# Performance work log

Hardware: AMD Instinct MI355X
Metric: run time of the kernel (lower is better)

The kernel has to match this reference:

```python
import jax, jax.numpy as jnp
import numpy as np

N_NODES = 100000
N_EDGES = 1600000
DIM = 128
BN_EPS = 1e-5


def setup_inputs() -> dict:
    key = jax.random.key(0)
    k1, k2, k3, k4 = jax.random.split(key, 4)
    scale = 1.0 / np.sqrt(DIM)
    return {
        "x": jax.random.normal(k1, (N_NODES, DIM), dtype=jnp.float32),
        "edge_index": jax.random.randint(k2, (2, N_EDGES), 0, N_NODES, dtype=jnp.int64),
        "W_l": jax.random.normal(k3, (DIM, DIM), dtype=jnp.float32) * scale,
        "b_l": jnp.zeros((DIM,), dtype=jnp.float32),
        "W_r": jax.random.normal(k4, (DIM, DIM), dtype=jnp.float32) * scale,
        "gamma": jnp.ones((DIM,), dtype=jnp.float32),
        "beta": jnp.zeros((DIM,), dtype=jnp.float32),
    }


def reference(x, edge_index, W_l, b_l, W_r, gamma, beta):
    n = x.shape[0]
    src, dst = edge_index[0], edge_index[1]
    # SAGEConv mean aggregation: gather source features, scatter-sum to dst, divide by degree
    agg = jax.ops.segment_sum(x[src], dst, num_segments=n)          # [N, d_in]
    deg = jax.ops.segment_sum(jnp.ones_like(src, dtype=x.dtype), dst, num_segments=n)
    mean = agg / jnp.maximum(deg, 1.0)[:, None]
    # lin_l(mean) + lin_r(x)  (bias lives in lin_l, PyG default)
    h = mean @ W_l + b_l + x @ W_r                                   # [N, d_out]
    # act -> BatchNorm1d (training mode, batch stats) -> dropout(p=0, identity)
    h = jax.nn.relu(h)
    mu = jnp.mean(h, axis=0)
    var = jnp.mean(jnp.square(h - mu), axis=0)                       # biased var, as torch BN
    h = (h - mu) * jax.lax.rsqrt(var + BN_EPS) * gamma + beta
    # residual
    return x + h
```

## Files before the change

### kernel.cpp

```cpp
#include <hip/hip_runtime.h>

#define DIM 128
#define BN_EPS 1e-5f
#define NB 32
#define NBK_MAX 512

typedef __attribute__((ext_vector_type(8))) short bf16x8;
typedef __attribute__((ext_vector_type(4))) float f32x4;

union B8 { uint4 u; bf16x8 s; };

__device__ __forceinline__ ushort f2bf(float f) {
    unsigned u = __float_as_uint(f);
    u += 0x7fffu + ((u >> 16) & 1u);
    return (ushort)(u >> 16);
}

__global__ void k_prep(const float4* __restrict__ x4, const float* __restrict__ Wl,
                       const float* __restrict__ Wr, const unsigned* __restrict__ eiu,
                       int* __restrict__ bcnt, uint2* __restrict__ xf8,
                       uint4* __restrict__ wpack, int nn, int ne, int PB, int WB) {
    __shared__ int nz;
    __shared__ int lh[NBK_MAX];
    int b = blockIdx.x;
    const int tid = threadIdx.x;

    if (b < PB) {
        const int t = b * 256 + tid;
        const int n8 = nn * DIM / 8;
        if (t < n8) {
            const float4 a = x4[2 * t], c = x4[2 * t + 1];
            int u0 = __builtin_amdgcn_cvt_pk_fp8_f32(a.x, a.y, 0, false);
            u0 = __builtin_amdgcn_cvt_pk_fp8_f32(a.z, a.w, u0, true);
            int u1 = __builtin_amdgcn_cvt_pk_fp8_f32(c.x, c.y, 0, false);
            u1 = __builtin_amdgcn_cvt_pk_fp8_f32(c.z, c.w, u1, true);
            xf8[t] = make_uint2((unsigned)u0, (unsigned)u1);
        }
        return;
    }
    b -= PB;
    if (b < WB) {
        const int t = b * 256 + tid;
        const int lane = t & 63, kk = (t >> 6) & 3, nt = (t >> 8) & 7, mat = t >> 11;
        const float* W = mat ? Wr : Wl;
        const int k0 = kk * 32 + (lane >> 4) * 8;
        const int n = nt * 16 + (lane & 15);
        ushort e[8];
#pragma unroll
        for (int j = 0; j < 8; ++j) e[j] = f2bf(W[(size_t)(k0 + j) * DIM + n]);
        uint4 o;
        o.x = ((unsigned)e[1] << 16) | e[0];
        o.y = ((unsigned)e[3] << 16) | e[2];
        o.z = ((unsigned)e[5] << 16) | e[4];
        o.w = ((unsigned)e[7] << 16) | e[6];
        wpack[t] = o;
        return;
    }
    b -= WB;
    const int nbk = (nn + 255) >> 8;
    for (int i = tid; i < nbk; i += 256) lh[i] = 0;
    if (tid == 0) nz = 0;
    __syncthreads();
    const int e0 = b * 4096;
    {
        int es = e0 + tid * 16;
        if (es >= ne) es = ne - 1;
        if (eiu[2 * (size_t)es + 1] != 0) atomicOr(&nz, 1);
    }
    __syncthreads();
    const int is64 = (nz == 0);
    for (int j = 0; j < 16; ++j) {
        const int e = e0 + j * 256 + tid;
        if (e < ne) {
            int dst;
            if (is64) dst = (int)((const long long*)eiu)[(size_t)ne + e];
            else      dst = ((const int*)eiu)[(size_t)ne + e];
            atomicAdd(&lh[dst >> 8], 1);
        }
    }
    __syncthreads();
    for (int i = tid; i < nbk; i += 256)
        if (lh[i]) atomicAdd(&bcnt[i], lh[i]);
}

__global__ __launch_bounds__(512) void k_scanb(const int* __restrict__ bcnt,
                                               int* __restrict__ bbase,
                                               int* __restrict__ cursor2, int nn, int ne) {
    __shared__ int sd[512];
    const int nbk = (nn + 255) >> 8;
    const int tid = threadIdx.x;
    const int v = (tid < nbk) ? bcnt[tid] : 0;
    sd[tid] = v;
    __syncthreads();
    for (int ofs = 1; ofs < 512; ofs <<= 1) {
        const int t = (tid >= ofs) ? sd[tid - ofs] : 0;
        __syncthreads();
        sd[tid] += t;
        __syncthreads();
    }
    if (tid < nbk) {
        const int ex = sd[tid] - v;
        bbase[tid] = ex;
        cursor2[tid] = ex;
    }
    if (tid == 0) bbase[nbk] = ne;
}

__global__ __launch_bounds__(256) void k_passA(const unsigned* __restrict__ eiu,
                                               int* __restrict__ cursor2,
                                               unsigned* __restrict__ pairbuf,
                                               int nn, int ne) {
    __shared__ int lh[NBK_MAX];
    __shared__ int gb[NBK_MAX];
    __shared__ int nz;
    const int nbk = (nn + 255) >> 8;
    const int tid = threadIdx.x;
    const int e0 = blockIdx.x * 4096;
    for (int i = tid; i < nbk; i += 256) lh[i] = 0;
    if (tid == 0) nz = 0;
    __syncthreads();
    {
        int es = e0 + tid * 16;
        if (es >= ne) es = ne - 1;
        if (eiu[2 * (size_t)es + 1] != 0) atomicOr(&nz, 1);
    }
    __syncthreads();
    const int is64 = (nz == 0);
    unsigned pay[16];
    int bkrank[16];
#pragma unroll
    for (int j = 0; j < 16; ++j) {
        const int e = e0 + j * 256 + tid;
        bkrank[j] = -1;
        if (e < ne) {
            int src, dst;
            if (is64) {
                const long long* p = (const long long*)eiu;
                src = (int)p[e];
                dst = (int)p[(size_t)ne + e];
            } else {
                const int* p = (const int*)eiu;
                src = p[e];
                dst = p[(size_t)ne + e];
            }
            const int bk = dst >> 8;
            const int rank = atomicAdd(&lh[bk], 1);
            bkrank[j] = (bk << 16) | rank;
            pay[j] = ((unsigned)(dst & 255) << 24) | (unsigned)src;
        }
    }
    __syncthreads();
    for (int i = tid; i < nbk; i += 256) {
        const int c = lh[i];
        gb[i] = c ? atomicAdd(&cursor2[i], c) : 0;
    }
    __syncthreads();
#pragma unroll
    for (int j = 0; j < 16; ++j) {
        if (bkrank[j] >= 0) {
            const int bk = bkrank[j] >> 16, rank = bkrank[j] & 0xFFFF;
            pairbuf[gb[bk] + rank] = pay[j];
        }
    }
}

__global__ __launch_bounds__(256) void k_passB(const unsigned* __restrict__ pairbuf,
                                               const int* __restrict__ bbase,
                                               int* __restrict__ off, int* __restrict__ cnt,
                                               int* __restrict__ srcbuf, int nn) {
    __shared__ int cl[256];
    __shared__ int sd[256];
    __shared__ int cur[256];
    const int tid = threadIdx.x;
    const int b = blockIdx.x;
    const int node0 = b << 8;
    const int e0 = bbase[b], e1 = bbase[b + 1];
    cl[tid] = 0;
    __syncthreads();
    for (int e = e0 + tid; e < e1; e += 256)
        atomicAdd(&cl[pairbuf[e] >> 24], 1);
    __syncthreads();
    const int v = cl[tid];
    sd[tid] = v;
    __syncthreads();
    for (int ofs = 1; ofs < 256; ofs <<= 1) {
        const int t = (tid >= ofs) ? sd[tid - ofs] : 0;
        __syncthreads();
        sd[tid] += t;
        __syncthreads();
    }
    const int ex = sd[tid] - v;
    cur[tid] = ex;
    const int node = node0 + tid;
    if (node < nn) {
        off[node] = e0 + ex;
        cnt[node] = v;
    }
    __syncthreads();
    for (int e = e0 + tid; e < e1; e += 256) {
        const unsigned p = pairbuf[e];
        const int pos = atomicAdd(&cur[p >> 24], 1);
        srcbuf[e0 + pos] = (int)(p & 0xFFFFFFu);
    }
}

__global__ __launch_bounds__(512, 4) void k_gemm(
    const float* __restrict__ x, const uint2* __restrict__ xf8,
    const uint4* __restrict__ wpack, const float* __restrict__ bl,
    const int* __restrict__ off, const int* __restrict__ cnt,
    const int* __restrict__ srcbuf,
    ushort* __restrict__ hout, float* __restrict__ ssum, float* __restrict__ ssq,
    int nn)
{
    __shared__ uint4 mean4[NB * 16];
    __shared__ uint4 xls4[NB * 16];
    __shared__ float red_sum[2][DIM];
    __shared__ float red_sq[2][DIM];
    unsigned* x_u = (unsigned*)xls4;

    const int tid = threadIdx.x;
    const int lane = tid & 63;
    const int w = tid >> 6;
    const int base = blockIdx.x * NB;
    const int g16 = lane >> 4;
    const int q = lane & 15;

    for (int n = 0; n < 4; ++n) {
        const int ln = w * 4 + n;
        const int node = base + ln;
        float acc[8];
#pragma unroll
        for (int j = 0; j < 8; ++j) acc[j] = 0.f;
        unsigned xw = 0;

        if (node < nn) {
            const float2 xv = *(const float2*)(x + (size_t)node * DIM + 2 * lane);
            xw = ((unsigned)f2bf(xv.y) << 16) | f2bf(xv.x);

            const int o = off[node];
            const int c = cnt[node];
            int e = 0;
            for (; e + 8 <= c; e += 8) {
                const int s0 = srcbuf[o + e + g16];
                const int s1 = srcbuf[o + e + 4 + g16];
                const uint2 v0 = xf8[(size_t)s0 * 16 + q];
                const uint2 v1 = xf8[(size_t)s1 * 16 + q];
                {
                    auto p0 = __builtin_amdgcn_cvt_pk_f32_fp8(v0.x, false);
                    auto p1 = __builtin_amdgcn_cvt_pk_f32_fp8(v0.x, true);
                    auto p2 = __builtin_amdgcn_cvt_pk_f32_fp8(v0.y, false);
                    auto p3 = __builtin_amdgcn_cvt_pk_f32_fp8(v0.y, true);
                    acc[0] += p0[0]; acc[1] += p0[1]; acc[2] += p1[0]; acc[3] += p1[1];
                    acc[4] += p2[0]; acc[5] += p2[1]; acc[6] += p3[0]; acc[7] += p3[1];
                }
                {
                    auto p0 = __builtin_amdgcn_cvt_pk_f32_fp8(v1.x, false);
                    auto p1 = __builtin_amdgcn_cvt_pk_f32_fp8(v1.x, true);
                    auto p2 = __builtin_amdgcn_cvt_pk_f32_fp8(v1.y, false);
                    auto p3 = __builtin_amdgcn_cvt_pk_f32_fp8(v1.y, true);
                    acc[0] += p0[0]; acc[1] += p0[1]; acc[2] += p1[0]; acc[3] += p1[1];
                    acc[4] += p2[0]; acc[5] += p2[1]; acc[6] += p3[0]; acc[7] += p3[1];
                }
            }
            for (; e + 4 <= c; e += 4) {
                const int s = srcbuf[o + e + g16];
                const uint2 v = xf8[(size_t)s * 16 + q];
                auto p0 = __builtin_amdgcn_cvt_pk_f32_fp8(v.x, false);
                auto p1 = __builtin_amdgcn_cvt_pk_f32_fp8(v.x, true);
                auto p2 = __builtin_amdgcn_cvt_pk_f32_fp8(v.y, false);
                auto p3 = __builtin_amdgcn_cvt_pk_f32_fp8(v.y, true);
                acc[0] += p0[0]; acc[1] += p0[1]; acc[2] += p1[0]; acc[3] += p1[1];
                acc[4] += p2[0]; acc[5] += p2[1]; acc[6] += p3[0]; acc[7] += p3[1];
            }
            const int rem = c - e;
            if (g16 < rem) {
                const int s = srcbuf[o + e + g16];
                const uint2 v = xf8[(size_t)s * 16 + q];
                auto p0 = __builtin_amdgcn_cvt_pk_f32_fp8(v.x, false);
                auto p1 = __builtin_amdgcn_cvt_pk_f32_fp8(v.x, true);
                auto p2 = __builtin_amdgcn_cvt_pk_f32_fp8(v.y, false);
                auto p3 = __builtin_amdgcn_cvt_pk_f32_fp8(v.y, true);
                acc[0] += p0[0]; acc[1] += p0[1]; acc[2] += p1[0]; acc[3] += p1[1];
                acc[4] += p2[0]; acc[5] += p2[1]; acc[6] += p3[0]; acc[7] += p3[1];
            }
#pragma unroll
            for (int j = 0; j < 8; ++j) {
                acc[j] += __shfl_xor(acc[j], 16);
                acc[j] += __shfl_xor(acc[j], 32);
            }
            const float r = 1.0f / fmaxf((float)c, 1.0f);
#pragma unroll
            for (int j = 0; j < 8; ++j) acc[j] *= r;
        }

        const int sw = (((lane >> 2) ^ (ln & 15)) << 2) | (lane & 3);
        x_u[ln * 64 + sw] = xw;
        if (lane < 16) {
            uint4 mp;
            mp.x = ((unsigned)f2bf(acc[1]) << 16) | f2bf(acc[0]);
            mp.y = ((unsigned)f2bf(acc[3]) << 16) | f2bf(acc[2]);
            mp.z = ((unsigned)f2bf(acc[5]) << 16) | f2bf(acc[4]);
            mp.w = ((unsigned)f2bf(acc[7]) << 16) | f2bf(acc[6]);
            mean4[ln * 16 + (q ^ (ln & 15))] = mp;
        }
    }
    __syncthreads();

    const int m = w & 1;
    const int nh = w >> 1;
    const int row16 = lane & 15;
    const int kgrp = lane >> 4;
    const int ln2 = m * 16 + row16;

    bf16x8 am[4], ax[4];
#pragma unroll
    for (int kk = 0; kk < 4; ++kk) {
        const int unit = (kk * 4 + kgrp) ^ row16;
        B8 va, vb;
        va.u = mean4[ln2 * 16 + unit];
        vb.u = xls4[ln2 * 16 + unit];
        am[kk] = va.s;
        ax[kk] = vb.s;
    }

    f32x4 acc[2];
#pragma unroll
    for (int j = 0; j < 2; ++j) {
        const float bv = bl[(nh * 2 + j) * 16 + row16];
        acc[j] = (f32x4){bv, bv, bv, bv};
    }

#pragma unroll
    for (int j = 0; j < 2; ++j) {
        const int nt = nh * 2 + j;
        const uint4* pl = wpack + (size_t)(nt * 4) * 64 + lane;
        const uint4* pr = wpack + (size_t)((8 + nt) * 4) * 64 + lane;
        B8 wl[4], wr[4];
#pragma unroll
        for (int kk = 0; kk < 4; ++kk) {
            wl[kk].u = pl[kk * 64];
            wr[kk].u = pr[kk * 64];
        }
#pragma unroll
        for (int kk = 0; kk < 4; ++kk)
            acc[j] = __builtin_amdgcn_mfma_f32_16x16x32_bf16(am[kk], wl[kk].s, acc[j], 0, 0, 0);
#pragma unroll
        for (int kk = 0; kk < 4; ++kk)
            acc[j] = __builtin_amdgcn_mfma_f32_16x16x32_bf16(ax[kk], wr[kk].s, acc[j], 0, 0, 0);
    }

#pragma unroll
    for (int j = 0; j < 2; ++j) {
        const int feat = (nh * 2 + j) * 16 + row16;
        float s = 0.f, sq = 0.f;
#pragma unroll
        for (int r = 0; r < 4; ++r) {
            const int node = base + m * 16 + kgrp * 4 + r;
            const float v = fmaxf(acc[j][r], 0.0f);
            if (node < nn) {
                hout[(size_t)node * DIM + feat] = f2bf(v);
                s += v;
                sq += v * v;
            }
        }
        s += __shfl_xor(s, 16);
        s += __shfl_xor(s, 32);
        sq += __shfl_xor(sq, 16);
        sq += __shfl_xor(sq, 32);
        if (lane < 16) {
            red_sum[m][feat] = s;
            red_sq[m][feat] = sq;
        }
    }
    __syncthreads();
    if (tid < DIM) {
        atomicAdd(&ssum[tid], red_sum[0][tid] + red_sum[1][tid]);
        atomicAdd(&ssq[tid], red_sq[0][tid] + red_sq[1][tid]);
    }
}

__global__ void k_finalize(const float* __restrict__ x, const uint4* __restrict__ h8,
                           const float* __restrict__ ssum, const float* __restrict__ ssq,
                           const float* __restrict__ gamma, const float* __restrict__ beta,
                           float* __restrict__ out, int nn)
{
    const float invN = 1.0f / (float)nn;
    const int total8 = nn * DIM / 8;
    const int stride = gridDim.x * blockDim.x;
    for (int i = blockIdx.x * blockDim.x + threadIdx.x; i < total8; i += stride) {
        const int f4 = 2 * (i & 15);
        const uint4 hv = h8[i];
        const float4 xa = ((const float4*)x)[2 * i];
        const float4 xb = ((const float4*)x)[2 * i + 1];
        const float4 s4a = ((const float4*)ssum)[f4], s4b = ((const float4*)ssum)[f4 + 1];
        const float4 q4a = ((const float4*)ssq)[f4], q4b = ((const float4*)ssq)[f4 + 1];
        const float4 g4a = ((const float4*)gamma)[f4], g4b = ((const float4*)gamma)[f4 + 1];
        const float4 b4a = ((const float4*)beta)[f4], b4b = ((const float4*)beta)[f4 + 1];
        float h[8];
        h[0] = __uint_as_float(hv.x << 16);
        h[1] = __uint_as_float(hv.x & 0xffff0000u);
        h[2] = __uint_as_float(hv.y << 16);
        h[3] = __uint_as_float(hv.y & 0xffff0000u);
        h[4] = __uint_as_float(hv.z << 16);
        h[5] = __uint_as_float(hv.z & 0xffff0000u);
        h[6] = __uint_as_float(hv.w << 16);
        h[7] = __uint_as_float(hv.w & 0xffff0000u);
        float4 oa, ob;
        {
            const float mu = s4a.x * invN, rs = rsqrtf(q4a.x * invN - mu * mu + BN_EPS);
            oa.x = xa.x + (h[0] - mu) * rs * g4a.x + b4a.x;
        }
        {
            const float mu = s4a.y * invN, rs = rsqrtf(q4a.y * invN - mu * mu + BN_EPS);
            oa.y = xa.y + (h[1] - mu) * rs * g4a.y + b4a.y;
        }
        {
            const float mu = s4a.z * invN, rs = rsqrtf(q4a.z * invN - mu * mu + BN_EPS);
            oa.z = xa.z + (h[2] - mu) * rs * g4a.z + b4a.z;
        }
        {
            const float mu = s4a.w * invN, rs = rsqrtf(q4a.w * invN - mu * mu + BN_EPS);
            oa.w = xa.w + (h[3] - mu) * rs * g4a.w + b4a.w;
        }
        {
            const float mu = s4b.x * invN, rs = rsqrtf(q4b.x * invN - mu * mu + BN_EPS);
            ob.x = xb.x + (h[4] - mu) * rs * g4b.x + b4b.x;
        }
        {
            const float mu = s4b.y * invN, rs = rsqrtf(q4b.y * invN - mu * mu + BN_EPS);
            ob.y = xb.y + (h[5] - mu) * rs * g4b.y + b4b.y;
        }
        {
            const float mu = s4b.z * invN, rs = rsqrtf(q4b.z * invN - mu * mu + BN_EPS);
            ob.z = xb.z + (h[6] - mu) * rs * g4b.z + b4b.z;
        }
        {
            const float mu = s4b.w * invN, rs = rsqrtf(q4b.w * invN - mu * mu + BN_EPS);
            ob.w = xb.w + (h[7] - mu) * rs * g4b.w + b4b.w;
        }
        ((float4*)out)[2 * i] = oa;
        ((float4*)out)[2 * i + 1] = ob;
    }
}

extern "C" void kernel_launch(void* const* d_in, const int* in_sizes, int n_in,
                              void* d_out, int out_size, void* d_ws, size_t ws_size,
                              hipStream_t stream) {
    const float* x     = (const float*)d_in[0];
    const void*  ei    = d_in[1];
    const float* Wl    = (const float*)d_in[2];
    const float* bl    = (const float*)d_in[3];
    const float* Wr    = (const float*)d_in[4];
    const float* gamma = (const float*)d_in[5];
    const float* beta  = (const float*)d_in[6];
    float* out = (float*)d_out;

    const int nn = in_sizes[0] / DIM;
    const int ne = in_sizes[1] / 2;
    const int nbk = (nn + 255) >> 8;

    int* ws = (int*)d_ws;
    int*   bcnt    = ws;
    float* ssum    = (float*)(ws + 512);
    float* ssq     = (float*)(ws + 640);
    int*   bbase   = ws + 768;
    int*   cursor2 = ws + 1280;
    int*   cnt     = ws + 1792;
    int*   off     = cnt + nn;
    size_t pos = 1792 + 2 * (size_t)nn;
    pos = (pos + 3) & ~(size_t)3;
    uint4* wpack  = (uint4*)(ws + pos);
    int*   srcbuf = (int*)(wpack + 4096);
    size_t p2 = (size_t)(srcbuf + ne - ws);
    p2 = (p2 + 3) & ~(size_t)3;
    uint2* xf8 = (uint2*)(ws + p2);
    unsigned* pairbuf = (unsigned*)(xf8 + (size_t)nn * 16);
    ushort*   hbuf    = (ushort*)pairbuf;

    hipMemsetAsync(d_ws, 0, 768 * sizeof(int), stream);

    const int PB = (nn * DIM / 8 + 255) / 256;
    const int WB = 16;
    const int HB = (ne + 4095) / 4096;
    k_prep<<<PB + WB + HB, 256, 0, stream>>>((const float4*)x, Wl, Wr,
                                             (const unsigned*)ei, bcnt, xf8, wpack,
                                             nn, ne, PB, WB);
    k_scanb<<<1, 512, 0, stream>>>(bcnt, bbase, cursor2, nn, ne);
    k_passA<<<(ne + 4095) / 4096, 256, 0, stream>>>((const unsigned*)ei, cursor2,
                                                    pairbuf, nn, ne);
    k_passB<<<nbk, 256, 0, stream>>>(pairbuf, bbase, off, cnt, srcbuf, nn);
    k_gemm<<<(nn + NB - 1) / NB, 512, 0, stream>>>(x, xf8, wpack, bl, off, cnt, srcbuf,
                                                   hbuf, ssum, ssq, nn);
    k_finalize<<<2048, 256, 0, stream>>>(x, (const uint4*)hbuf, ssum, ssq, gamma, beta,
                                         out, nn);
}
```

Measured before the change: 194.2 us.

## Assign one node per 16-lane group in aggregation and per-node finalize grid

The neighbour-gather phase of k_gemm now maps each 16-lane quarter-wave to its own node, so a wave handles four nodes at once. Previously the whole wave walked one node at a time, with the four quarters splitting its edges and a cross-lane shuffle reduction at the end. This drops the shuffle reduction and the serial four-node loop, but spreads uneven degrees across lanes in the same wave, so divergence rises. The x tile is packed to bf16 in uint4 chunks per lane, and k_finalize switches from a grid-stride loop to one block per 32-node tile.

```diff
diff --git a/kernel.cpp b/kernel.cpp
--- a/kernel.cpp
+++ b/kernel.cpp
@@ -205,7 +205,7 @@
 }
 
 __global__ __launch_bounds__(512, 4) void k_gemm(
-    const float* __restrict__ x, const uint2* __restrict__ xf8,
+    const float4* __restrict__ x4g, const uint2* __restrict__ xf8,
     const uint4* __restrict__ wpack, const float* __restrict__ bl,
     const int* __restrict__ off, const int* __restrict__ cnt,
     const int* __restrict__ srcbuf,
@@ -216,55 +216,56 @@
     __shared__ uint4 xls4[NB * 16];
     __shared__ float red_sum[2][DIM];
     __shared__ float red_sq[2][DIM];
-    unsigned* x_u = (unsigned*)xls4;
 
     const int tid = threadIdx.x;
     const int lane = tid & 63;
     const int w = tid >> 6;
     const int base = blockIdx.x * NB;
-    const int g16 = lane >> 4;
+    const int g = lane >> 4;
     const int q = lane & 15;
 
-    for (int n = 0; n < 4; ++n) {
-        const int ln = w * 4 + n;
+    {
+        const int ln = w * 4 + g;
         const int node = base + ln;
         float acc[8];
 #pragma unroll
         for (int j = 0; j < 8; ++j) acc[j] = 0.f;
-        unsigned xw = 0;
+        uint4 xp = make_uint4(0, 0, 0, 0);
 
         if (node < nn) {
-            const float2 xv = *(const float2*)(x + (size_t)node * DIM + 2 * lane);
-            xw = ((unsigned)f2bf(xv.y) << 16) | f2bf(xv.x);
+            const float4 xa = x4g[(size_t)node * 32 + 2 * q];
+            const float4 xb = x4g[(size_t)node * 32 + 2 * q + 1];
+            xp.x = ((unsigned)f2bf(xa.y) << 16) | f2bf(xa.x);
+            xp.y = ((unsigned)f2bf(xa.w) << 16) | f2bf(xa.z);
+            xp.z = ((unsigned)f2bf(xb.y) << 16) | f2bf(xb.x);
+            xp.w = ((unsigned)f2bf(xb.w) << 16) | f2bf(xb.z);
 
             const int o = off[node];
             const int c = cnt[node];
             int e = 0;
-            for (; e + 8 <= c; e += 8) {
-                const int s0 = srcbuf[o + e + g16];
-                const int s1 = srcbuf[o + e + 4 + g16];
-                const uint2 v0 = xf8[(size_t)s0 * 16 + q];
-                const uint2 v1 = xf8[(size_t)s1 * 16 + q];
-                {
-                    auto p0 = __builtin_amdgcn_cvt_pk_f32_fp8(v0.x, false);
-                    auto p1 = __builtin_amdgcn_cvt_pk_f32_fp8(v0.x, true);
-                    auto p2 = __builtin_amdgcn_cvt_pk_f32_fp8(v0.y, false);
-                    auto p3 = __builtin_amdgcn_cvt_pk_f32_fp8(v0.y, true);
-                    acc[0] += p0[0]; acc[1] += p0[1]; acc[2] += p1[0]; acc[3] += p1[1];
-                    acc[4] += p2[0]; acc[5] += p2[1]; acc[6] += p3[0]; acc[7] += p3[1];
-                }
-                {
-                    auto p0 = __builtin_amdgcn_cvt_pk_f32_fp8(v1.x, false);
-                    auto p1 = __builtin_amdgcn_cvt_pk_f32_fp8(v1.x, true);
-                    auto p2 = __builtin_amdgcn_cvt_pk_f32_fp8(v1.y, false);
-                    auto p3 = __builtin_amdgcn_cvt_pk_f32_fp8(v1.y, true);
+            for (; e + 4 <= c; e += 4) {
+                const int s0 = srcbuf[o + e + 0];
+                const int s1 = srcbuf[o + e + 1];
+                const int s2 = srcbuf[o + e + 2];
+                const int s3 = srcbuf[o + e + 3];
+                const uint2 v0 = xf8[(unsigned)(s0 * 16 + q)];
+                const uint2 v1 = xf8[(unsigned)(s1 * 16 + q)];
+                const uint2 v2 = xf8[(unsigned)(s2 * 16 + q)];
+                const uint2 v3 = xf8[(unsigned)(s3 * 16 + q)];
+#pragma unroll
+                for (int k = 0; k < 4; ++k) {
+                    const uint2 v = (k == 0) ? v0 : (k == 1) ? v1 : (k == 2) ? v2 : v3;
+                    auto p0 = __builtin_amdgcn_cvt_pk_f32_fp8(v.x, false);
+                    auto p1 = __builtin_amdgcn_cvt_pk_f32_fp8(v.x, true);
+                    auto p2 = __builtin_amdgcn_cvt_pk_f32_fp8(v.y, false);
+                    auto p3 = __builtin_amdgcn_cvt_pk_f32_fp8(v.y, true);
                     acc[0] += p0[0]; acc[1] += p0[1]; acc[2] += p1[0]; acc[3] += p1[1];
                     acc[4] += p2[0]; acc[5] += p2[1]; acc[6] += p3[0]; acc[7] += p3[1];
                 }
             }
-            for (; e + 4 <= c; e += 4) {
-                const int s = srcbuf[o + e + g16];
-                const uint2 v = xf8[(size_t)s * 16 + q];
+            for (; e < c; ++e) {
+                const int s = srcbuf[o + e];
+                const uint2 v = xf8[(unsigned)(s * 16 + q)];
                 auto p0 = __builtin_amdgcn_cvt_pk_f32_fp8(v.x, false);
                 auto p1 = __builtin_amdgcn_cvt_pk_f32_fp8(v.x, true);
                 auto p2 = __builtin_amdgcn_cvt_pk_f32_fp8(v.y, false);
@@ -272,37 +273,19 @@
                 acc[0] += p0[0]; acc[1] += p0[1]; acc[2] += p1[0]; acc[3] += p1[1];
                 acc[4] += p2[0]; acc[5] += p2[1]; acc[6] += p3[0]; acc[7] += p3[1];
             }
-            const int rem = c - e;
-            if (g16 < rem) {
-                const int s = srcbuf[o + e + g16];
-                const uint2 v = xf8[(size_t)s * 16 + q];
-                auto p0 = __builtin_amdgcn_cvt_pk_f32_fp8(v.x, false);
-                auto p1 = __builtin_amdgcn_cvt_pk_f32_fp8(v.x, true);
-                auto p2 = __builtin_amdgcn_cvt_pk_f32_fp8(v.y, false);
-                auto p3 = __builtin_amdgcn_cvt_pk_f32_fp8(v.y, true);
-                acc[0] += p0[0]; acc[1] += p0[1]; acc[2] += p1[0]; acc[3] += p1[1];
-                acc[4] += p2[0]; acc[5] += p2[1]; acc[6] += p3[0]; acc[7] += p3[1];
-            }
-#pragma unroll
-            for (int j = 0; j < 8; ++j) {
-                acc[j] += __shfl_xor(acc[j], 16);
-                acc[j] += __shfl_xor(acc[j], 32);
-            }
             const float r = 1.0f / fmaxf((float)c, 1.0f);
 #pragma unroll
             for (int j = 0; j < 8; ++j) acc[j] *= r;
         }
 
-        const int sw = (((lane >> 2) ^ (ln & 15)) << 2) | (lane & 3);
-        x_u[ln * 64 + sw] = xw;
-        if (lane < 16) {
-            uint4 mp;
-            mp.x = ((unsigned)f2bf(acc[1]) << 16) | f2bf(acc[0]);
-            mp.y = ((unsigned)f2bf(acc[3]) << 16) | f2bf(acc[2]);
-            mp.z = ((unsigned)f2bf(acc[5]) << 16) | f2bf(acc[4]);
-            mp.w = ((unsigned)f2bf(acc[7]) << 16) | f2bf(acc[6]);
-            mean4[ln * 16 + (q ^ (ln & 15))] = mp;
-        }
+        uint4 mp;
+        mp.x = ((unsigned)f2bf(acc[1]) << 16) | f2bf(acc[0]);
+        mp.y = ((unsigned)f2bf(acc[3]) << 16) | f2bf(acc[2]);
+        mp.z = ((unsigned)f2bf(acc[5]) << 16) | f2bf(acc[4]);
+        mp.w = ((unsigned)f2bf(acc[7]) << 16) | f2bf(acc[6]);
+        const int slot = q ^ (ln & 15);
+        mean4[ln * 16 + slot] = mp;
+        xls4[ln * 16 + slot] = xp;
     }
     __syncthreads();
 
@@ -379,68 +362,68 @@
     }
 }
 
-__global__ void k_finalize(const float* __restrict__ x, const uint4* __restrict__ h8,
-                           const float* __restrict__ ssum, const float* __restrict__ ssq,
-                           const float* __restrict__ gamma, const float* __restrict__ beta,
-                           float* __restrict__ out, int nn)
+__global__ __launch_bounds__(512) void k_finalize(
+    const float4* __restrict__ x4, const uint4* __restrict__ h4,
+    const float* __restrict__ ssum, const float* __restrict__ ssq,
+    const float* __restrict__ gamma, const float* __restrict__ beta,
+    float4* __restrict__ out4, int nn)
 {
     const float invN = 1.0f / (float)nn;
-    const int total8 = nn * DIM / 8;
-    const int stride = gridDim.x * blockDim.x;
-    for (int i = blockIdx.x * blockDim.x + threadIdx.x; i < total8; i += stride) {
-        const int f4 = 2 * (i & 15);
-        const uint4 hv = h8[i];
-        const float4 xa = ((const float4*)x)[2 * i];
-        const float4 xb = ((const float4*)x)[2 * i + 1];
-        const float4 s4a = ((const float4*)ssum)[f4], s4b = ((const float4*)ssum)[f4 + 1];
-        const float4 q4a = ((const float4*)ssq)[f4], q4b = ((const float4*)ssq)[f4 + 1];
-        const float4 g4a = ((const float4*)gamma)[f4], g4b = ((const float4*)gamma)[f4 + 1];
-        const float4 b4a = ((const float4*)beta)[f4], b4b = ((const float4*)beta)[f4 + 1];
-        float h[8];
-        h[0] = __uint_as_float(hv.x << 16);
-        h[1] = __uint_as_float(hv.x & 0xffff0000u);
-        h[2] = __uint_as_float(hv.y << 16);
-        h[3] = __uint_as_float(hv.y & 0xffff0000u);
-        h[4] = __uint_as_float(hv.z << 16);
-        h[5] = __uint_as_float(hv.z & 0xffff0000u);
-        h[6] = __uint_as_float(hv.w << 16);
-        h[7] = __uint_as_float(hv.w & 0xffff0000u);
-        float4 oa, ob;
-        {
-            const float mu = s4a.x * invN, rs = rsqrtf(q4a.x * invN - mu * mu + BN_EPS);
-            oa.x = xa.x + (h[0] - mu) * rs * g4a.x + b4a.x;
-        }
-        {
-            const float mu = s4a.y * invN, rs = rsqrtf(q4a.y * invN - mu * mu + BN_EPS);
-            oa.y = xa.y + (h[1] - mu) * rs * g4a.y + b4a.y;
-        }
-        {
-            const float mu = s4a.z * invN, rs = rsqrtf(q4a.z * invN - mu * mu + BN_EPS);
-            oa.z = xa.z + (h[2] - mu) * rs * g4a.z + b4a.z;
-        }
-        {
-            const float mu = s4a.w * invN, rs = rsqrtf(q4a.w * invN - mu * mu + BN_EPS);
-            oa.w = xa.w + (h[3] - mu) * rs * g4a.w + b4a.w;
-        }
-        {
-            const float mu = s4b.x * invN, rs = rsqrtf(q4b.x * invN - mu * mu + BN_EPS);
-            ob.x = xb.x + (h[4] - mu) * rs * g4b.x + b4b.x;
-        }
-        {
-            const float mu = s4b.y * invN, rs = rsqrtf(q4b.y * invN - mu * mu + BN_EPS);
-            ob.y = xb.y + (h[5] - mu) * rs * g4b.y + b4b.y;
-        }
-        {
-            const float mu = s4b.z * invN, rs = rsqrtf(q4b.z * invN - mu * mu + BN_EPS);
-            ob.z = xb.z + (h[6] - mu) * rs * g4b.z + b4b.z;
-        }
-        {
-            const float mu = s4b.w * invN, rs = rsqrtf(q4b.w * invN - mu * mu + BN_EPS);
-            ob.w = xb.w + (h[7] - mu) * rs * g4b.w + b4b.w;
-        }
-        ((float4*)out)[2 * i] = oa;
-        ((float4*)out)[2 * i + 1] = ob;
-    }
+    const int tid = threadIdx.x;
+    const int node = blockIdx.x * 32 + (tid >> 4);
+    const int q = tid & 15;
+    if (node >= nn) return;
+    const uint4 hv = h4[(size_t)node * 16 + q];
+    const float4 xa = x4[(size_t)node * 32 + 2 * q];
+    const float4 xb = x4[(size_t)node * 32 + 2 * q + 1];
+    const float4 s4a = ((const float4*)ssum)[2 * q], s4b = ((const float4*)ssum)[2 * q + 1];
+    const float4 q4a = ((const float4*)ssq)[2 * q], q4b = ((const float4*)ssq)[2 * q + 1];
+    const float4 g4a = ((const float4*)gamma)[2 * q], g4b = ((const float4*)gamma)[2 * q + 1];
+    const float4 b4a = ((const float4*)beta)[2 * q], b4b = ((const float4*)beta)[2 * q + 1];
+    float h[8];
+    h[0] = __uint_as_float(hv.x << 16);
+    h[1] = __uint_as_float(hv.x & 0xffff0000u);
+    h[2] = __uint_as_float(hv.y << 16);
+    h[3] = __uint_as_float(hv.y & 0xffff0000u);
+    h[4] = __uint_as_float(hv.z << 16);
+    h[5] = __uint_as_float(hv.z & 0xffff0000u);
+    h[6] = __uint_as_float(hv.w << 16);
+    h[7] = __uint_as_float(hv.w & 0xffff0000u);
+    float4 oa, ob;
+    {
+        const float mu = s4a.x * invN, rs = rsqrtf(q4a.x * invN - mu * mu + BN_EPS);
+        oa.x = xa.x + (h[0] - mu) * rs * g4a.x + b4a.x;
+    }
+    {
+        const float mu = s4a.y * invN, rs = rsqrtf(q4a.y * invN - mu * mu + BN_EPS);
+        oa.y = xa.y + (h[1] - mu) * rs * g4a.y + b4a.y;
+    }
+    {
+        const float mu = s4a.z * invN, rs = rsqrtf(q4a.z * invN - mu * mu + BN_EPS);
+        oa.z = xa.z + (h[2] - mu) * rs * g4a.z + b4a.z;
+    }
+    {
+        const float mu = s4a.w * invN, rs = rsqrtf(q4a.w * invN - mu * mu + BN_EPS);
+        oa.w = xa.w + (h[3] - mu) * rs * g4a.w + b4a.w;
+    }
+    {
+        const float mu = s4b.x * invN, rs = rsqrtf(q4b.x * invN - mu * mu + BN_EPS);
+        ob.x = xb.x + (h[4] - mu) * rs * g4b.x + b4b.x;
+    }
+    {
+        const float mu = s4b.y * invN, rs = rsqrtf(q4b.y * invN - mu * mu + BN_EPS);
+        ob.y = xb.y + (h[5] - mu) * rs * g4b.y + b4b.y;
+    }
+    {
+        const float mu = s4b.z * invN, rs = rsqrtf(q4b.z * invN - mu * mu + BN_EPS);
+        ob.z = xb.z + (h[6] - mu) * rs * g4b.z + b4b.z;
+    }
+    {
+        const float mu = s4b.w * invN, rs = rsqrtf(q4b.w * invN - mu * mu + BN_EPS);
+        ob.w = xb.w + (h[7] - mu) * rs * g4b.w + b4b.w;
+    }
+    out4[(size_t)node * 32 + 2 * q] = oa;
+    out4[(size_t)node * 32 + 2 * q + 1] = ob;
 }
 
 extern "C" void kernel_launch(void* const* d_in, const int* in_sizes, int n_in,
@@ -489,8 +472,9 @@
     k_passA<<<(ne + 4095) / 4096, 256, 0, stream>>>((const unsigned*)ei, cursor2,
                                                     pairbuf, nn, ne);
     k_passB<<<nbk, 256, 0, stream>>>(pairbuf, bbase, off, cnt, srcbuf, nn);
-    k_gemm<<<(nn + NB - 1) / NB, 512, 0, stream>>>(x, xf8, wpack, bl, off, cnt, srcbuf,
-                                                   hbuf, ssum, ssq, nn);
-    k_finalize<<<2048, 256, 0, stream>>>(x, (const uint4*)hbuf, ssum, ssq, gamma, beta,
-                                         out, nn);
-}
+    const int ntile = (nn + NB - 1) / NB;
+    k_gemm<<<ntile, 512, 0, stream>>>((const float4*)x, xf8, wpack, bl, off, cnt,
+                                      srcbuf, hbuf, ssum, ssq, nn);
+    k_finalize<<<ntile, 512, 0, stream>>>((const float4*)x, (const uint4*)hbuf,
+                                          ssum, ssq, gamma, beta, (float4*)out, nn);
+}
```

Measured after the change: 187.3 us. 1.04x faster.
